# Kernel tuning notes

Measured on AMD Instinct MI355X. Metric: run time of the kernel, lower is better.

Reference implementation:

```python
import jax, jax.numpy as jnp
import numpy as np

N_NODES = 100000
MAX_DEG = 64
NODE_DIM = 256
V = 8192
NUM_SAMPLES = 16


def setup_inputs() -> dict:
    key = jax.random.key(0)
    k1, k2, k3, k4 = jax.random.split(key, 4)
    ids = jax.random.randint(k1, (V,), 0, N_NODES, dtype=jnp.int32)
    adj_info = jax.random.randint(k2, (N_NODES, MAX_DEG), 0, N_NODES, dtype=jnp.int32)
    features = jax.random.normal(k3, (N_NODES, NODE_DIM), dtype=jnp.float32)
    W = jax.random.normal(k4, (NODE_DIM, NODE_DIM), dtype=jnp.float32) * 0.05
    b = jnp.zeros((NODE_DIM,), dtype=jnp.float32)
    return {"ids": ids, "adj_info": adj_info, "features": features, "W": W, "b": b,
            "num_samples": NUM_SAMPLES}


def reference(ids, adj_info, features, W, b, num_samples):
    n_nodes, neig_num = adj_info.shape
    group_dim = neig_num // num_samples
    K = group_dim * num_samples  # tf.slice to a multiple of num_samples
    v = ids.shape[0]

    adj_lists = adj_info[ids][:, :K]                     # [V, K] neighbor ids
    v_f = features[ids]                                  # [V, d]
    n_f = features[adj_lists]                            # [V, K, d]

    # linear sampler branch: dense(v_f) then matmul with neighbor feats, relu
    l = v_f @ W + b                                      # [V, d]
    scores = jax.nn.relu(jnp.einsum('vd,vkd->vk', l, n_f))  # [V, K]

    # grouped argmin: pick one neighbor per group of group_dim
    scores = scores.reshape(v, num_samples, group_dim)   # [V, S, G]
    idx_y = jnp.argmin(scores, axis=-1).astype(jnp.int32)  # [V, S]
    idx_y = idx_y + (jnp.arange(num_samples, dtype=jnp.int32) * group_dim)[None, :]

    sel = jnp.take_along_axis(adj_lists, idx_y, axis=1)  # [V, S]

    # count non-padding neighbors (padding sentinel = n_nodes - 1)
    nonpad = jnp.where(sel == n_nodes - 1,
                       jnp.zeros(sel.shape, jnp.float32),
                       jnp.ones(sel.shape, jnp.float32))
    numnz = nonpad.sum(axis=1)                           # [V]
    att = jnp.ones(sel.shape, jnp.float32)
    return sel, att, numnz, numnz
```

## Files before the change

### kernel.cpp

```cpp
#include <hip/hip_runtime.h>
#include <hip/hip_bf16.h>

#define N_NODES   100000
#define MAX_DEG   64
#define NODE_DIM  256
#define NUM_V     8192
#define NSAMP     16
#define GROUP_DIM 4
#define SENTINEL  (N_NODES - 1)

#define BM 64
#define BN 64
#define BK 16

__global__ __launch_bounds__(256) void gemm_l_kernel(
    const int* __restrict__ ids,
    const float* __restrict__ features,
    const float* __restrict__ W,
    const float* __restrict__ bias,
    float* __restrict__ l_out) {
  __shared__ float As[BK][BM];
  __shared__ float Ws[BK][BN];
  __shared__ int   nid_s[BM];

  const int tid  = threadIdx.x;
  const int row0 = blockIdx.x * BM;
  const int col0 = blockIdx.y * BN;

  if (tid < BM) nid_s[tid] = ids[row0 + tid];
  __syncthreads();

  const int tx = tid & 15;
  const int ty = tid >> 4;

  const int am = tid >> 2;
  const int ak = (tid & 3) * 4;
  const int wk = tid >> 4;
  const int wn = (tid & 15) * 4;

  const size_t a_base = (size_t)nid_s[am] * NODE_DIM + ak;

  float acc[4][4] = {};

  for (int k0 = 0; k0 < NODE_DIM; k0 += BK) {
    const float4 av = *reinterpret_cast<const float4*>(&features[a_base + k0]);
    As[ak + 0][am] = av.x;
    As[ak + 1][am] = av.y;
    As[ak + 2][am] = av.z;
    As[ak + 3][am] = av.w;
    *reinterpret_cast<float4*>(&Ws[wk][wn]) = *reinterpret_cast<const float4*>(
        &W[(size_t)(k0 + wk) * NODE_DIM + col0 + wn]);
    __syncthreads();

#pragma unroll
    for (int k = 0; k < BK; ++k) {
      const float4 ra = *reinterpret_cast<const float4*>(&As[k][ty * 4]);
      const float4 rb = *reinterpret_cast<const float4*>(&Ws[k][tx * 4]);
      const float a[4] = {ra.x, ra.y, ra.z, ra.w};
      const float b[4] = {rb.x, rb.y, rb.z, rb.w};
#pragma unroll
      for (int i = 0; i < 4; ++i)
#pragma unroll
        for (int j = 0; j < 4; ++j) acc[i][j] += a[i] * b[j];
    }
    __syncthreads();
  }

  const float4 bv =
      *reinterpret_cast<const float4*>(&bias[col0 + tx * 4]);
#pragma unroll
  for (int i = 0; i < 4; ++i) {
    const int m = row0 + ty * 4 + i;
    float4 o;
    o.x = acc[i][0] + bv.x;
    o.y = acc[i][1] + bv.y;
    o.z = acc[i][2] + bv.z;
    o.w = acc[i][3] + bv.w;
    *reinterpret_cast<float4*>(&l_out[(size_t)m * NODE_DIM + col0 + tx * 4]) = o;
  }
}

__global__ __launch_bounds__(256) void sampler_kernel(
    const int* __restrict__ ids,
    const int* __restrict__ adj,
    const float* __restrict__ features,
    const float* __restrict__ l,
    float* __restrict__ out_sel,
    float* __restrict__ out_att,
    float* __restrict__ out_nz1,
    float* __restrict__ out_nz2) {
  __shared__ float l_s[NODE_DIM];
  __shared__ int   adj_s[MAX_DEG];
  __shared__ float nz_s[NSAMP];

  const int v   = blockIdx.x;
  const int tid = threadIdx.x;
  const int nid = ids[v];

  l_s[tid] = l[(size_t)v * NODE_DIM + tid];
  if (tid < MAX_DEG) adj_s[tid] = adj[(size_t)nid * MAX_DEG + tid];
  __syncthreads();

  const int wave = tid >> 6;
  const int lane = tid & 63;
  const int q    = lane >> 2;
  const int sub  = lane & 3;
  const int k    = wave * 16 + q;

  const int nb = adj_s[k];
  const float* __restrict__ rowp = features + (size_t)nb * NODE_DIM + sub * 4;
  const float* __restrict__ lp   = l_s + sub * 4;

  float p = 0.0f;
#pragma unroll
  for (int c = 0; c < 16; ++c) {
    const float4 f  = *reinterpret_cast<const float4*>(rowp + c * 16);
    const float4 lv = *reinterpret_cast<const float4*>(lp + c * 16);
    p += f.x * lv.x + f.y * lv.y + f.z * lv.z + f.w * lv.w;
  }
  p += __shfl_xor(p, 1, 64);
  p += __shfl_xor(p, 2, 64);
  float s = p > 0.0f ? p : 0.0f;

  int g = q & 3;
  {
    float os = __shfl_xor(s, 4, 64);
    int   og = __shfl_xor(g, 4, 64);
    if (os < s || (os == s && og < g)) { s = os; g = og; }
    os = __shfl_xor(s, 8, 64);
    og = __shfl_xor(g, 8, 64);
    if (os < s || (os == s && og < g)) { s = os; g = og; }
  }

  if ((lane & 15) == 0) {
    const int gl    = lane >> 4;
    const int s_idx = wave * 4 + gl;
    const int selid = adj_s[s_idx * GROUP_DIM + g];
    out_sel[(size_t)v * NSAMP + s_idx] = (float)selid;
    out_att[(size_t)v * NSAMP + s_idx] = 1.0f;
    nz_s[s_idx] = (selid == SENTINEL) ? 0.0f : 1.0f;
  }
  __syncthreads();

  if (tid == 0) {
    float nz = 0.0f;
#pragma unroll
    for (int t = 0; t < NSAMP; ++t) nz += nz_s[t];
    out_nz1[v] = nz;
    out_nz2[v] = nz;
  }
}

extern "C" void kernel_launch(void* const* d_in, const int* in_sizes, int n_in,
                              void* d_out, int out_size, void* d_ws,
                              size_t ws_size, hipStream_t stream) {
  const int*   ids      = (const int*)d_in[0];
  const int*   adj      = (const int*)d_in[1];
  const float* features = (const float*)d_in[2];
  const float* W        = (const float*)d_in[3];
  const float* bias     = (const float*)d_in[4];

  float* l_ws = (float*)d_ws;

  float* out     = (float*)d_out;
  float* out_sel = out;
  float* out_att = out + (size_t)NUM_V * NSAMP;
  float* out_nz1 = out + (size_t)2 * NUM_V * NSAMP;
  float* out_nz2 = out_nz1 + NUM_V;

  gemm_l_kernel<<<dim3(NUM_V / BM, NODE_DIM / BN), 256, 0, stream>>>(
      ids, features, W, bias, l_ws);
  sampler_kernel<<<NUM_V, 256, 0, stream>>>(ids, adj, features, l_ws, out_sel,
                                            out_att, out_nz1, out_nz2);
}
```

Measured before the change: 239.9 us.

## Fuse dense projection into sampler kernel, computing four rows per block

Removes the separate tiled GEMM kernel and the intermediate l buffer. Each block now computes the projection for four vertices directly from W and the gathered feature rows, then runs the neighbour scoring and grouped argmin for those vertices one at a time. This saves a launch and the global round trip of l. In exchange every block streams all of W with little register reuse, and the per-block serial loop reduces gather parallelism.

```diff
diff --git a/kernel.cpp b/kernel.cpp
--- a/kernel.cpp
+++ b/kernel.cpp
@@ -8,146 +8,111 @@
 #define NSAMP     16
 #define GROUP_DIM 4
 #define SENTINEL  (N_NODES - 1)
+#define VPB       4
 
-#define BM 64
-#define BN 64
-#define BK 16
-
-__global__ __launch_bounds__(256) void gemm_l_kernel(
+__global__ __launch_bounds__(256) void sampler_fused_kernel(
     const int* __restrict__ ids,
+    const int* __restrict__ adj,
     const float* __restrict__ features,
     const float* __restrict__ W,
     const float* __restrict__ bias,
-    float* __restrict__ l_out) {
-  __shared__ float As[BK][BM];
-  __shared__ float Ws[BK][BN];
-  __shared__ int   nid_s[BM];
-
-  const int tid  = threadIdx.x;
-  const int row0 = blockIdx.x * BM;
-  const int col0 = blockIdx.y * BN;
-
-  if (tid < BM) nid_s[tid] = ids[row0 + tid];
-  __syncthreads();
-
-  const int tx = tid & 15;
-  const int ty = tid >> 4;
-
-  const int am = tid >> 2;
-  const int ak = (tid & 3) * 4;
-  const int wk = tid >> 4;
-  const int wn = (tid & 15) * 4;
-
-  const size_t a_base = (size_t)nid_s[am] * NODE_DIM + ak;
-
-  float acc[4][4] = {};
-
-  for (int k0 = 0; k0 < NODE_DIM; k0 += BK) {
-    const float4 av = *reinterpret_cast<const float4*>(&features[a_base + k0]);
-    As[ak + 0][am] = av.x;
-    As[ak + 1][am] = av.y;
-    As[ak + 2][am] = av.z;
-    As[ak + 3][am] = av.w;
-    *reinterpret_cast<float4*>(&Ws[wk][wn]) = *reinterpret_cast<const float4*>(
-        &W[(size_t)(k0 + wk) * NODE_DIM + col0 + wn]);
-    __syncthreads();
-
-#pragma unroll
-    for (int k = 0; k < BK; ++k) {
-      const float4 ra = *reinterpret_cast<const float4*>(&As[k][ty * 4]);
-      const float4 rb = *reinterpret_cast<const float4*>(&Ws[k][tx * 4]);
-      const float a[4] = {ra.x, ra.y, ra.z, ra.w};
-      const float b[4] = {rb.x, rb.y, rb.z, rb.w};
-#pragma unroll
-      for (int i = 0; i < 4; ++i)
-#pragma unroll
-        for (int j = 0; j < 4; ++j) acc[i][j] += a[i] * b[j];
-    }
-    __syncthreads();
-  }
-
-  const float4 bv =
-      *reinterpret_cast<const float4*>(&bias[col0 + tx * 4]);
-#pragma unroll
-  for (int i = 0; i < 4; ++i) {
-    const int m = row0 + ty * 4 + i;
-    float4 o;
-    o.x = acc[i][0] + bv.x;
-    o.y = acc[i][1] + bv.y;
-    o.z = acc[i][2] + bv.z;
-    o.w = acc[i][3] + bv.w;
-    *reinterpret_cast<float4*>(&l_out[(size_t)m * NODE_DIM + col0 + tx * 4]) = o;
-  }
-}
-
-__global__ __launch_bounds__(256) void sampler_kernel(
-    const int* __restrict__ ids,
-    const int* __restrict__ adj,
-    const float* __restrict__ features,
-    const float* __restrict__ l,
     float* __restrict__ out_sel,
     float* __restrict__ out_att,
     float* __restrict__ out_nz1,
     float* __restrict__ out_nz2) {
-  __shared__ float l_s[NODE_DIM];
+  __shared__ float l_s[VPB][NODE_DIM];
   __shared__ int   adj_s[MAX_DEG];
   __shared__ float nz_s[NSAMP];
 
-  const int v   = blockIdx.x;
   const int tid = threadIdx.x;
-  const int nid = ids[v];
+  const int v0  = blockIdx.x * VPB;
 
-  l_s[tid] = l[(size_t)v * NODE_DIM + tid];
-  if (tid < MAX_DEG) adj_s[tid] = adj[(size_t)nid * MAX_DEG + tid];
+  const int nid0 = ids[v0 + 0];
+  const int nid1 = ids[v0 + 1];
+  const int nid2 = ids[v0 + 2];
+  const int nid3 = ids[v0 + 3];
+
+  {
+    const float* __restrict__ f0 = features + (size_t)nid0 * NODE_DIM;
+    const float* __restrict__ f1 = features + (size_t)nid1 * NODE_DIM;
+    const float* __restrict__ f2 = features + (size_t)nid2 * NODE_DIM;
+    const float* __restrict__ f3 = features + (size_t)nid3 * NODE_DIM;
+
+    float a0 = 0.0f, a1 = 0.0f, a2 = 0.0f, a3 = 0.0f;
+#pragma unroll 8
+    for (int k = 0; k < NODE_DIM; ++k) {
+      const float wv = W[(size_t)k * NODE_DIM + tid];
+      a0 = fmaf(f0[k], wv, a0);
+      a1 = fmaf(f1[k], wv, a1);
+      a2 = fmaf(f2[k], wv, a2);
+      a3 = fmaf(f3[k], wv, a3);
+    }
+    const float bv = bias[tid];
+    l_s[0][tid] = a0 + bv;
+    l_s[1][tid] = a1 + bv;
+    l_s[2][tid] = a2 + bv;
+    l_s[3][tid] = a3 + bv;
+  }
   __syncthreads();
 
   const int wave = tid >> 6;
   const int lane = tid & 63;
   const int q    = lane >> 2;
   const int sub  = lane & 3;
-  const int k    = wave * 16 + q;
+  const int kidx = wave * 16 + q;
 
-  const int nb = adj_s[k];
-  const float* __restrict__ rowp = features + (size_t)nb * NODE_DIM + sub * 4;
-  const float* __restrict__ lp   = l_s + sub * 4;
+  const int nids[VPB] = {nid0, nid1, nid2, nid3};
 
-  float p = 0.0f;
+  for (int i = 0; i < VPB; ++i) {
+    const int v = v0 + i;
+
+    if (tid < MAX_DEG) adj_s[tid] = adj[(size_t)nids[i] * MAX_DEG + tid];
+    __syncthreads();
+
+    const int nb = adj_s[kidx];
+    const float* __restrict__ rowp =
+        features + (size_t)nb * NODE_DIM + sub * 4;
+    const float* __restrict__ lp = &l_s[i][sub * 4];
+
+    float p = 0.0f;
 #pragma unroll
-  for (int c = 0; c < 16; ++c) {
-    const float4 f  = *reinterpret_cast<const float4*>(rowp + c * 16);
-    const float4 lv = *reinterpret_cast<const float4*>(lp + c * 16);
-    p += f.x * lv.x + f.y * lv.y + f.z * lv.z + f.w * lv.w;
-  }
-  p += __shfl_xor(p, 1, 64);
-  p += __shfl_xor(p, 2, 64);
-  float s = p > 0.0f ? p : 0.0f;
+    for (int c = 0; c < 16; ++c) {
+      const float4 f  = *reinterpret_cast<const float4*>(rowp + c * 16);
+      const float4 lv = *reinterpret_cast<const float4*>(lp + c * 16);
+      p += f.x * lv.x + f.y * lv.y + f.z * lv.z + f.w * lv.w;
+    }
+    p += __shfl_xor(p, 1, 64);
+    p += __shfl_xor(p, 2, 64);
+    float s = p > 0.0f ? p : 0.0f;
 
-  int g = q & 3;
-  {
-    float os = __shfl_xor(s, 4, 64);
-    int   og = __shfl_xor(g, 4, 64);
-    if (os < s || (os == s && og < g)) { s = os; g = og; }
-    os = __shfl_xor(s, 8, 64);
-    og = __shfl_xor(g, 8, 64);
-    if (os < s || (os == s && og < g)) { s = os; g = og; }
-  }
+    int g = q & 3;
+    {
+      float os = __shfl_xor(s, 4, 64);
+      int   og = __shfl_xor(g, 4, 64);
+      if (os < s || (os == s && og < g)) { s = os; g = og; }
+      os = __shfl_xor(s, 8, 64);
+      og = __shfl_xor(g, 8, 64);
+      if (os < s || (os == s && og < g)) { s = os; g = og; }
+    }
 
-  if ((lane & 15) == 0) {
-    const int gl    = lane >> 4;
-    const int s_idx = wave * 4 + gl;
-    const int selid = adj_s[s_idx * GROUP_DIM + g];
-    out_sel[(size_t)v * NSAMP + s_idx] = (float)selid;
-    out_att[(size_t)v * NSAMP + s_idx] = 1.0f;
-    nz_s[s_idx] = (selid == SENTINEL) ? 0.0f : 1.0f;
-  }
-  __syncthreads();
+    if ((lane & 15) == 0) {
+      const int gl    = lane >> 4;
+      const int s_idx = wave * 4 + gl;
+      const int selid = adj_s[s_idx * GROUP_DIM + g];
+      out_sel[(size_t)v * NSAMP + s_idx] = (float)selid;
+      out_att[(size_t)v * NSAMP + s_idx] = 1.0f;
+      nz_s[s_idx] = (selid == SENTINEL) ? 0.0f : 1.0f;
+    }
+    __syncthreads();
 
-  if (tid == 0) {
-    float nz = 0.0f;
+    if (tid == 0) {
+      float nz = 0.0f;
 #pragma unroll
-    for (int t = 0; t < NSAMP; ++t) nz += nz_s[t];
-    out_nz1[v] = nz;
-    out_nz2[v] = nz;
+      for (int t = 0; t < NSAMP; ++t) nz += nz_s[t];
+      out_nz1[v] = nz;
+      out_nz2[v] = nz;
+    }
+    __syncthreads();
   }
 }
 
@@ -160,16 +125,12 @@
   const float* W        = (const float*)d_in[3];
   const float* bias     = (const float*)d_in[4];
 
-  float* l_ws = (float*)d_ws;
-
   float* out     = (float*)d_out;
   float* out_sel = out;
   float* out_att = out + (size_t)NUM_V * NSAMP;
   float* out_nz1 = out + (size_t)2 * NUM_V * NSAMP;
   float* out_nz2 = out_nz1 + NUM_V;
 
-  gemm_l_kernel<<<dim3(NUM_V / BM, NODE_DIM / BN), 256, 0, stream>>>(
-      ids, features, W, bias, l_ws);
-  sampler_kernel<<<NUM_V, 256, 0, stream>>>(ids, adj, features, l_ws, out_sel,
-                                            out_att, out_nz1, out_nz2);
+  sampler_fused_kernel<<<NUM_V / VPB, 256, 0, stream>>>(
+      ids, adj, features, W, bias, out_sel, out_att, out_nz1, out_nz2);
 }
```

Result: slower. 251.1 us (+4.7%).
